# Kernel tuning notes

Hardware: AMD Instinct MI355X
Metric: run time of the kernel (lower is better)

Reference implementation:

```python
import jax, jax.numpy as jnp
import numpy as np

N_NODES = 50000
N_EDGES = 1600000
IN_F = 128
HID = 256
DROP_P = 0.6  # keep prob 0.4


def setup_inputs() -> dict:
    key = jax.random.key(0)
    ks = jax.random.split(key, 8)
    s_in = 1.0 / np.sqrt(IN_F)
    s_h = 1.0 / np.sqrt(HID)
    return {
        "x": jax.random.normal(ks[0], (N_NODES, IN_F), dtype=jnp.float32),
        "edge_index": jax.random.randint(ks[1], (2, N_EDGES), 0, N_NODES, dtype=jnp.int64),
        "w_rel0": jax.random.normal(ks[2], (IN_F, HID), dtype=jnp.float32) * s_in,
        "b_rel0": jax.random.normal(ks[3], (HID,), dtype=jnp.float32) * s_in,
        "w_root0": jax.random.normal(ks[4], (IN_F, HID), dtype=jnp.float32) * s_in,
        "w_rel1": jax.random.normal(ks[5], (HID, HID), dtype=jnp.float32) * s_h,
        "b_rel1": jax.random.normal(ks[6], (HID,), dtype=jnp.float32) * s_h,
        "w_root1": jax.random.normal(ks[7], (HID, HID), dtype=jnp.float32) * s_h,
    }


def _dropout(h, key, p):
    keep = 1.0 - p
    mask = jax.random.bernoulli(key, keep, h.shape)
    return jnp.where(mask, h / keep, 0.0).astype(h.dtype)


def _graph_conv(h, src, dst, n_nodes, w_rel, b_rel, w_root):
    # PyG GraphConv: out_i = lin_rel(sum_{j->i} x_j) + lin_root(x_i)
    agg = jax.ops.segment_sum(h[src], dst, num_segments=n_nodes)  # [N, F]
    return agg @ w_rel + b_rel + h @ w_root


def reference(x, edge_index, w_rel0, b_rel0, w_root0, w_rel1, b_rel1, w_root1):
    src, dst = edge_index[0], edge_index[1]  # flow: source -> target
    n = x.shape[0]
    dkey = jax.random.key(42)
    k0, k1 = jax.random.split(dkey)

    h = _dropout(x, k0, DROP_P)
    h = _graph_conv(h, src, dst, n, w_rel0, b_rel0, w_root0)
    h = jax.nn.relu(h)

    h = _dropout(h, k1, DROP_P)
    h = _graph_conv(h, src, dst, n, w_rel1, b_rel1, w_root1)
    h = jax.nn.relu(h)
    return h
```

## Files before the change

### kernel.cpp

```cpp
#include <hip/hip_runtime.h>
#include <cstdint>

typedef unsigned int u32;
typedef unsigned short u16;

#define NN 50000
#define NE 1600000
#define LDA0 288

#define NPART 196
#define SPAN1 2048
#define NB1 ((NE + SPAN1 - 1) / SPAN1)

typedef __bf16 bf16x8 __attribute__((ext_vector_type(8)));
typedef float f32x16 __attribute__((ext_vector_type(16)));

__host__ __device__ static inline void tf2x32(u32 ka, u32 kb, u32 x0, u32 x1,
                                              u32& o0, u32& o1) {
  const u32 kc = ka ^ kb ^ 0x1BD11BDAu;
  u32 v0 = x0 + ka, v1 = x1 + kb;
#define TFR(r) { v0 += v1; v1 = (v1 << (r)) | (v1 >> (32 - (r))); v1 ^= v0; }
  TFR(13) TFR(15) TFR(26) TFR(6)   v0 += kb; v1 += kc + 1u;
  TFR(17) TFR(29) TFR(16) TFR(24)  v0 += kc; v1 += ka + 2u;
  TFR(13) TFR(15) TFR(26) TFR(6)   v0 += ka; v1 += kb + 3u;
  TFR(17) TFR(29) TFR(16) TFR(24)  v0 += kb; v1 += kc + 4u;
  TFR(13) TFR(15) TFR(26) TFR(6)   v0 += kc; v1 += ka + 5u;
#undef TFR
  o0 = v0; o1 = v1;
}

__device__ static inline u32 tfbits(u32 ka, u32 kb, u32 j) {
  u32 o0, o1;
  tf2x32(ka, kb, 0u, j, o0, o1);
  return o0 ^ o1;
}

__device__ static inline float u01(u32 bits) {
  return __uint_as_float((bits >> 9) | 0x3f800000u) - 1.0f;
}
__device__ static inline u16 f2bf(float f) {
  u32 u = __float_as_uint(f);
  return (u16)((u + 0x7fffu + ((u >> 16) & 1u)) >> 16);
}
__device__ static inline float bflo(u32 w) { return __uint_as_float(w << 16); }
__device__ static inline float bfhi(u32 w) { return __uint_as_float(w & 0xffff0000u); }

#define PRO_DROP 12500
#define PRO_COMP 18750
#define PRO_TOT  19518

__global__ __launch_bounds__(256) void prologue_kernel(
    const float* __restrict__ x, const int* __restrict__ ei,
    const float* __restrict__ wr0, const float* __restrict__ wroot0,
    const float* __restrict__ wr1, const float* __restrict__ wroot1,
    u16* __restrict__ A0, u32* __restrict__ epack,
    u16* __restrict__ Wt0, u16* __restrict__ Wt1,
    u32 ka, u32 kb) {
  int bid = blockIdx.x;
  int tid = threadIdx.x;
  if (bid < PRO_DROP) {
    int j0 = (bid * 256 + tid) * 2;
    float v0 = (u01(tfbits(ka, kb, (u32)j0)) < 0.4f) ? x[j0] * 2.5f : 0.0f;
    float v1 = (u01(tfbits(ka, kb, (u32)j0 + 1u)) < 0.4f) ? x[j0 + 1] * 2.5f : 0.0f;
    int r = j0 >> 7, c = j0 & 127;
    *(u32*)&A0[r * LDA0 + 128 + c] = (u32)f2bf(v0) | ((u32)f2bf(v1) << 16);
  } else if (bid < PRO_COMP) {
    __shared__ int s_nz;
    if (tid == 0) s_nz = 0;
    __syncthreads();
    if (ei[2 * (tid & 127) + 1] != 0) s_nz = 1;
    __syncthreads();
    int f = s_nz ? 0 : 1;
    int i = (bid - PRO_DROP) * 256 + tid;
    int s = f ? ei[2 * (size_t)i] : ei[i];
    int d = f ? ei[2 * ((size_t)NE + i)] : ei[(size_t)NE + i];
    epack[i] = (u32)s | ((u32)d << 16);
  } else {
    int i = (bid - PRO_COMP) * 256 + tid;
    if (i < 256 * 256) {
      int n = i >> 8, k = i & 255;
      float v = (k < 128) ? wr0[k * 256 + n] : wroot0[(k - 128) * 256 + n];
      Wt0[n * 256 + k] = f2bf(v);
    }
    int j = i - 256 * 256;
    if (j >= 0 && j < 256 * 512) {
      int n = j >> 9, k = j & 511;
      float v = (k < 256) ? wr1[k * 256 + n] : wroot1[(k - 256) * 256 + n];
      Wt1[n * 512 + k] = f2bf(v);
    }
  }
}

__global__ __launch_bounds__(256) void p1_count_kernel(const u32* __restrict__ epack,
                                                       u32* __restrict__ pcnt) {
  __shared__ u32 cnt[NPART];
  int b = blockIdx.x, t = threadIdx.x;
  if (t < NPART) cnt[t] = 0;
  __syncthreads();
  int base = b * SPAN1;
#pragma unroll
  for (int k = 0; k < SPAN1 / 256; k++) {
    int i = base + k * 256 + t;
    if (i < NE) atomicAdd(&cnt[epack[i] >> 24], 1);
  }
  __syncthreads();
  if (t < NPART) pcnt[b * NPART + t] = cnt[t];
}

__global__ __launch_bounds__(256) void p1b_scan_kernel(const u32* __restrict__ pcnt,
                                                       u32* __restrict__ pofs,
                                                       u32* __restrict__ psize) {
  __shared__ u32 sc[256];
  int p = blockIdx.x, t = threadIdx.x;
  u32 val[4];
  u32 tsum = 0;
#pragma unroll
  for (int k = 0; k < 4; k++) {
    int b = t * 4 + k;
    val[k] = (b < NB1) ? pcnt[b * NPART + p] : 0;
    tsum += val[k];
  }
  sc[t] = tsum;
  __syncthreads();
#pragma unroll
  for (int d = 1; d < 256; d <<= 1) {
    u32 x = (t >= d) ? sc[t - d] : 0;
    __syncthreads();
    sc[t] += x;
    __syncthreads();
  }
  u32 run = sc[t] - tsum;
#pragma unroll
  for (int k = 0; k < 4; k++) {
    int b = t * 4 + k;
    if (b < NB1) { pofs[p * NB1 + b] = run; run += val[k]; }
  }
  if (t == 255) psize[p] = sc[255];
}

__global__ __launch_bounds__(256) void p1c_base_kernel(const u32* __restrict__ psize,
                                                       u32* __restrict__ pbase) {
  __shared__ u32 sc[256];
  int t = threadIdx.x;
  u32 v = (t < NPART) ? psize[t] : 0;
  sc[t] = v;
  __syncthreads();
#pragma unroll
  for (int d = 1; d < 256; d <<= 1) {
    u32 x = (t >= d) ? sc[t - d] : 0;
    __syncthreads();
    sc[t] += x;
    __syncthreads();
  }
  if (t < NPART) pbase[t] = sc[t] - v;
  if (t == NPART - 1) pbase[NPART] = sc[t];
}

__global__ __launch_bounds__(256) void p1d_pscatter_kernel(const u32* __restrict__ epack,
                                                           const u32* __restrict__ pofs,
                                                           const u32* __restrict__ pbase,
                                                           u32* __restrict__ part_buf) {
  __shared__ u32 cur[NPART];
  int b = blockIdx.x, t = threadIdx.x;
  if (t < NPART) cur[t] = pbase[t] + pofs[t * NB1 + b];
  __syncthreads();
  int base = b * SPAN1;
#pragma unroll
  for (int k = 0; k < SPAN1 / 256; k++) {
    int i = base + k * 256 + t;
    if (i < NE) {
      u32 v = epack[i];
      u32 p = v >> 24;
      u32 slot = atomicAdd(&cur[p], 1);
      part_buf[slot] = (v & 0xffffu) | (((v >> 16) & 255u) << 16);
    }
  }
}

__global__ __launch_bounds__(256) void p2_sort_kernel(const u32* __restrict__ part_buf,
                                                      const u32* __restrict__ pbase,
                                                      int* __restrict__ offs,
                                                      u16* __restrict__ ssrc) {
  __shared__ u32 cnt[256], sc[256], cur[256];
  int p = blockIdx.x, t = threadIdx.x;
  u32 pb = pbase[p];
  int sz = (int)(pbase[p + 1] - pb);
  cnt[t] = 0;
  __syncthreads();
  for (int i = t; i < sz; i += 256)
    atomicAdd(&cnt[(part_buf[pb + i] >> 16) & 255u], 1);
  __syncthreads();
  u32 val = cnt[t];
  sc[t] = val;
  __syncthreads();
#pragma unroll
  for (int d = 1; d < 256; d <<= 1) {
    u32 x = (t >= d) ? sc[t - d] : 0;
    __syncthreads();
    sc[t] += x;
    __syncthreads();
  }
  u32 excl = sc[t] - val;
  int node = (p << 8) + t;
  if (node <= NN) offs[node] = (int)(pb + excl);
  cur[t] = excl;
  __syncthreads();
  for (int i = t; i < sz; i += 256) {
    u32 v = part_buf[pb + i];
    u32 slot = atomicAdd(&cur[(v >> 16) & 255u], 1);
    ssrc[pb + slot] = (u16)(v & 0xffffu);
  }
}

#define ACC8Q(V, S) { acc[0] += rintf(bflo(V.x) * S); acc[1] += rintf(bfhi(V.x) * S); \
                      acc[2] += rintf(bflo(V.y) * S); acc[3] += rintf(bfhi(V.y) * S); \
                      acc[4] += rintf(bflo(V.z) * S); acc[5] += rintf(bfhi(V.z) * S); \
                      acc[6] += rintf(bflo(V.w) * S); acc[7] += rintf(bfhi(V.w) * S); }

__global__ __launch_bounds__(256) void agg0_kernel(u16* __restrict__ A0,
                                                   const int* __restrict__ offs,
                                                   const u16* __restrict__ ssrc) {
  const float S = 8192.0f, INV = 1.0f / 8192.0f;
  int node = blockIdx.x * 4 + (threadIdx.x >> 6);
  int lane = threadIdx.x & 63;
  int l15 = lane & 15, eh = lane >> 4;
  int s = offs[node], e = offs[node + 1];
  float acc[8] = {0.f, 0.f, 0.f, 0.f, 0.f, 0.f, 0.f, 0.f};
  int i = s;
  for (; i + 16 <= e; i += 16) {
    uint4 w0 = *(const uint4*)&A0[(int)ssrc[i + eh] * LDA0 + 128 + l15 * 8];
    uint4 w1 = *(const uint4*)&A0[(int)ssrc[i + 4 + eh] * LDA0 + 128 + l15 * 8];
    uint4 w2 = *(const uint4*)&A0[(int)ssrc[i + 8 + eh] * LDA0 + 128 + l15 * 8];
    uint4 w3 = *(const uint4*)&A0[(int)ssrc[i + 12 + eh] * LDA0 + 128 + l15 * 8];
    ACC8Q(w0, S); ACC8Q(w1, S); ACC8Q(w2, S); ACC8Q(w3, S);
  }
  for (; i + 4 <= e; i += 4) {
    uint4 w0 = *(const uint4*)&A0[(int)ssrc[i + eh] * LDA0 + 128 + l15 * 8];
    ACC8Q(w0, S);
  }
  if (i + eh < e) {
    uint4 w0 = *(const uint4*)&A0[(int)ssrc[i + eh] * LDA0 + 128 + l15 * 8];
    ACC8Q(w0, S);
  }
#pragma unroll
  for (int j = 0; j < 8; j++) {
    acc[j] += __shfl_xor(acc[j], 16);
    acc[j] += __shfl_xor(acc[j], 32);
  }
  if (lane < 16) {
    uint4 o;
    o.x = (u32)f2bf(acc[0] * INV) | ((u32)f2bf(acc[1] * INV) << 16);
    o.y = (u32)f2bf(acc[2] * INV) | ((u32)f2bf(acc[3] * INV) << 16);
    o.z = (u32)f2bf(acc[4] * INV) | ((u32)f2bf(acc[5] * INV) << 16);
    o.w = (u32)f2bf(acc[6] * INV) | ((u32)f2bf(acc[7] * INV) << 16);
    *(uint4*)&A0[node * LDA0 + l15 * 8] = o;
  }
}

__global__ __launch_bounds__(256) void agg1_kernel(u16* __restrict__ A1,
                                                   const int* __restrict__ offs,
                                                   const u16* __restrict__ ssrc,
                                                   int node0) {
  const float S = 256.0f, INV = 1.0f / 256.0f;
  int node = node0 + blockIdx.x * 4 + (threadIdx.x >> 6);
  int lane = threadIdx.x & 63;
  int l31 = lane & 31, eh = lane >> 5;
  int s = offs[node], e = offs[node + 1];
  float acc[8] = {0.f, 0.f, 0.f, 0.f, 0.f, 0.f, 0.f, 0.f};
  int i = s;
  for (; i + 8 <= e; i += 8) {
    uint4 w0 = *(const uint4*)&A1[(int)ssrc[i + eh] * 512 + 256 + l31 * 8];
    uint4 w1 = *(const uint4*)&A1[(int)ssrc[i + 2 + eh] * 512 + 256 + l31 * 8];
    uint4 w2 = *(const uint4*)&A1[(int)ssrc[i + 4 + eh] * 512 + 256 + l31 * 8];
    uint4 w3 = *(const uint4*)&A1[(int)ssrc[i + 6 + eh] * 512 + 256 + l31 * 8];
    ACC8Q(w0, S); ACC8Q(w1, S); ACC8Q(w2, S); ACC8Q(w3, S);
  }
  for (; i + 2 <= e; i += 2) {
    uint4 w0 = *(const uint4*)&A1[(int)ssrc[i + eh] * 512 + 256 + l31 * 8];
    ACC8Q(w0, S);
  }
  if (i + eh < e) {
    uint4 w0 = *(const uint4*)&A1[(int)ssrc[i + eh] * 512 + 256 + l31 * 8];
    ACC8Q(w0, S);
  }
#pragma unroll
  for (int j = 0; j < 8; j++) acc[j] += __shfl_xor(acc[j], 32);
  if (eh == 0) {
    uint4 o;
    o.x = (u32)f2bf(acc[0] * INV) | ((u32)f2bf(acc[1] * INV) << 16);
    o.y = (u32)f2bf(acc[2] * INV) | ((u32)f2bf(acc[3] * INV) << 16);
    o.z = (u32)f2bf(acc[4] * INV) | ((u32)f2bf(acc[5] * INV) << 16);
    o.w = (u32)f2bf(acc[6] * INV) | ((u32)f2bf(acc[7] * INV) << 16);
    *(uint4*)&A1[node * 512 + l31 * 8] = o;
  }
}

template <int K, int LDA, bool DROP>
__global__ __launch_bounds__(512) void gemm_kernel(const u16* __restrict__ A,
                                                   const u16* __restrict__ Wt,
                                                   const float* __restrict__ bias,
                                                   u16* __restrict__ outB,
                                                   float* __restrict__ outF,
                                                   u32 ka, u32 kb) {
  constexpr int BK = 64;
  constexpr int LDP = BK + 8;
  __shared__ __align__(16) u16 Alds[128 * LDP];
  __shared__ __align__(16) u16 Blds[256 * LDP];
  const int tid = threadIdx.x;
  const int row0 = blockIdx.x * 128;
  const int lane = tid & 63;
  const int wid = tid >> 6;
  const int wr = wid & 3;
  const int wc = wid >> 2;
  const int l31 = lane & 31;
  const int lkhi = (lane >> 5) * 8;

  f32x16 acc[4];
#pragma unroll
  for (int i = 0; i < 4; i++)
#pragma unroll
    for (int j = 0; j < 16; j++) acc[i][j] = 0.0f;

#pragma unroll
  for (int kc = 0; kc < K / BK; kc++) {
#pragma unroll
    for (int i = 0; i < 2; i++) {
      int id = tid + i * 512;
      int r = id >> 3, c = id & 7;
      int rg = row0 + r; if (rg > NN - 1) rg = NN - 1;
      *(uint4*)&Alds[r * LDP + c * 8] =
          *(const uint4*)&A[(size_t)rg * LDA + kc * BK + c * 8];
    }
#pragma unroll
    for (int i = 0; i < 4; i++) {
      int id = tid + i * 512;
      int r = id >> 3, c = id & 7;
      *(uint4*)&Blds[r * LDP + c * 8] =
          *(const uint4*)&Wt[(size_t)r * K + kc * BK + c * 8];
    }
    __syncthreads();
#pragma unroll
    for (int ks = 0; ks < BK / 16; ks++) {
      bf16x8 a = *(const bf16x8*)&Alds[(wr * 32 + l31) * LDP + ks * 16 + lkhi];
#pragma unroll
      for (int ct = 0; ct < 4; ct++) {
        bf16x8 b = *(const bf16x8*)&Blds[(wc * 128 + ct * 32 + l31) * LDP + ks * 16 + lkhi];
        acc[ct] = __builtin_amdgcn_mfma_f32_32x32x16_bf16(a, b, acc[ct], 0, 0, 0);
      }
    }
    __syncthreads();
  }

#pragma unroll
  for (int ct = 0; ct < 4; ct++) {
    int col = wc * 128 + ct * 32 + l31;
    float bv = bias[col];
#pragma unroll
    for (int r = 0; r < 16; r++) {
      int row = row0 + wr * 32 + (r & 3) + 8 * (r >> 2) + 4 * (lane >> 5);
      if (row < NN) {
        float v = acc[ct][r] + bv;
        v = fmaxf(v, 0.0f);
        if constexpr (DROP) {
          u32 j = (u32)row * 256u + (u32)col;
          v = (u01(tfbits(ka, kb, j)) < 0.4f) ? v * 2.5f : 0.0f;
          outB[(size_t)row * 512 + 256 + col] = f2bf(v);
        } else {
          outF[(size_t)row * 256 + col] = v;
        }
      }
    }
  }
}

extern "C" void kernel_launch(void* const* d_in, const int* in_sizes, int n_in,
                              void* d_out, int out_size, void* d_ws, size_t ws_size,
                              hipStream_t stream) {
  (void)in_sizes; (void)n_in; (void)out_size; (void)ws_size;
  const float* x       = (const float*)d_in[0];
  const int*   ei      = (const int*)d_in[1];
  const float* w_rel0  = (const float*)d_in[2];
  const float* b_rel0  = (const float*)d_in[3];
  const float* w_root0 = (const float*)d_in[4];
  const float* w_rel1  = (const float*)d_in[5];
  const float* b_rel1  = (const float*)d_in[6];
  const float* w_root1 = (const float*)d_in[7];
  float* out = (float*)d_out;

  u32 k0a, k0b, k1a, k1b;
  tf2x32(0u, 42u, 0u, 0u, k0a, k0b);
  tf2x32(0u, 42u, 0u, 1u, k1a, k1b);

  uint8_t* p = (uint8_t*)d_ws;
  auto alloc = [&](size_t bytes) {
    uint8_t* r = p;
    p += (bytes + 255) & ~(size_t)255;
    return r;
  };
  u16* A0       = (u16*)alloc((size_t)NN * LDA0 * 2);
  u16* Wt0      = (u16*)alloc(256 * 256 * 2);
  u16* Wt1      = (u16*)alloc(256 * 512 * 2);
  int* offs     = (int*)alloc((size_t)(NN + 1) * 4);
  u16* ssrc     = (u16*)alloc((size_t)NE * 2);
  u32* epack    = (u32*)alloc((size_t)NE * 4);
  u32* pcnt     = (u32*)alloc((size_t)NB1 * NPART * 4);
  u32* pofs     = (u32*)alloc((size_t)NPART * NB1 * 4);
  u32* psize    = (u32*)alloc((size_t)NPART * 4);
  u32* pbase    = (u32*)alloc((size_t)(NPART + 1) * 4);
  u32* part_buf = (u32*)alloc((size_t)NE * 4);

  u16* A1 = (u16*)d_out;

  const int GEMM_NB = (NN + 127) / 128;

  prologue_kernel<<<PRO_TOT, 256, 0, stream>>>(x, ei, w_rel0, w_root0, w_rel1,
                                               w_root1, A0, epack, Wt0, Wt1,
                                               k0a, k0b);
  p1_count_kernel<<<NB1, 256, 0, stream>>>(epack, pcnt);
  p1b_scan_kernel<<<NPART, 256, 0, stream>>>(pcnt, pofs, psize);
  p1c_base_kernel<<<1, 256, 0, stream>>>(psize, pbase);
  p1d_pscatter_kernel<<<NB1, 256, 0, stream>>>(epack, pofs, pbase, part_buf);
  p2_sort_kernel<<<NPART, 256, 0, stream>>>(part_buf, pbase, offs, ssrc);
  agg0_kernel<<<12500, 256, 0, stream>>>(A0, offs, ssrc);
  gemm_kernel<256, LDA0, true><<<GEMM_NB, 512, 0, stream>>>(A0, Wt0, b_rel0, A1, nullptr, k1a, k1b);
  agg1_kernel<<<6250, 256, 0, stream>>>(A1, offs, ssrc, 0);
  agg1_kernel<<<6250, 256, 0, stream>>>(A1, offs, ssrc, 25000);
  gemm_kernel<512, 512, false><<<GEMM_NB, 512, 0, stream>>>(A1, Wt1, b_rel1, nullptr, out, 0u, 0u);
}
```

Measured before the change: 308.0 us.

## Fold partition base scan into consumers, merge agg1 launches, widen GEMM row tile

The separate single-block base-scan kernel is removed. Instead, the scatter kernel and the sort kernel each recompute the prefix scan of partition sizes in shared memory, which drops one launch and its serial dependency at the cost of a redundant 256-wide scan in every block. The two half-range agg1 launches become one launch over all nodes. The GEMM tile grows from 128 to 256 rows, with each of the 8 waves now computing 32 rows across all 256 columns; this halves how often the weight tile is reloaded but cuts the grid to 196 blocks, which may underfill the GPU's CUs.

```diff
diff --git a/kernel.cpp b/kernel.cpp
--- a/kernel.cpp
+++ b/kernel.cpp
@@ -138,10 +138,13 @@
   if (t == 255) psize[p] = sc[255];
 }
 
-__global__ __launch_bounds__(256) void p1c_base_kernel(const u32* __restrict__ psize,
-                                                       u32* __restrict__ pbase) {
+__global__ __launch_bounds__(256) void p1d_pscatter_kernel(const u32* __restrict__ epack,
+                                                           const u32* __restrict__ pofs,
+                                                           const u32* __restrict__ psize,
+                                                           u32* __restrict__ part_buf) {
   __shared__ u32 sc[256];
-  int t = threadIdx.x;
+  __shared__ u32 cur[NPART];
+  int b = blockIdx.x, t = threadIdx.x;
   u32 v = (t < NPART) ? psize[t] : 0;
   sc[t] = v;
   __syncthreads();
@@ -152,41 +155,43 @@
     sc[t] += x;
     __syncthreads();
   }
-  if (t < NPART) pbase[t] = sc[t] - v;
-  if (t == NPART - 1) pbase[NPART] = sc[t];
-}
-
-__global__ __launch_bounds__(256) void p1d_pscatter_kernel(const u32* __restrict__ epack,
-                                                           const u32* __restrict__ pofs,
-                                                           const u32* __restrict__ pbase,
-                                                           u32* __restrict__ part_buf) {
-  __shared__ u32 cur[NPART];
-  int b = blockIdx.x, t = threadIdx.x;
-  if (t < NPART) cur[t] = pbase[t] + pofs[t * NB1 + b];
+  if (t < NPART) cur[t] = (sc[t] - v) + pofs[t * NB1 + b];
   __syncthreads();
   int base = b * SPAN1;
 #pragma unroll
   for (int k = 0; k < SPAN1 / 256; k++) {
     int i = base + k * 256 + t;
     if (i < NE) {
-      u32 v = epack[i];
-      u32 p = v >> 24;
+      u32 e = epack[i];
+      u32 p = e >> 24;
       u32 slot = atomicAdd(&cur[p], 1);
-      part_buf[slot] = (v & 0xffffu) | (((v >> 16) & 255u) << 16);
+      part_buf[slot] = (e & 0xffffu) | (((e >> 16) & 255u) << 16);
     }
   }
 }
 
 __global__ __launch_bounds__(256) void p2_sort_kernel(const u32* __restrict__ part_buf,
-                                                      const u32* __restrict__ pbase,
+                                                      const u32* __restrict__ psize,
                                                       int* __restrict__ offs,
                                                       u16* __restrict__ ssrc) {
-  __shared__ u32 cnt[256], sc[256], cur[256];
+  __shared__ u32 sc[256], cnt[256], cur[256];
+  __shared__ u32 s_pb;
   int p = blockIdx.x, t = threadIdx.x;
-  u32 pb = pbase[p];
-  int sz = (int)(pbase[p + 1] - pb);
+  u32 v = (t < NPART) ? psize[t] : 0;
+  sc[t] = v;
+  __syncthreads();
+#pragma unroll
+  for (int d = 1; d < 256; d <<= 1) {
+    u32 x = (t >= d) ? sc[t - d] : 0;
+    __syncthreads();
+    sc[t] += x;
+    __syncthreads();
+  }
+  if (t == p) s_pb = sc[t] - v;
   cnt[t] = 0;
   __syncthreads();
+  u32 pb = s_pb;
+  int sz = (int)psize[p];
   for (int i = t; i < sz; i += 256)
     atomicAdd(&cnt[(part_buf[pb + i] >> 16) & 255u], 1);
   __syncthreads();
@@ -206,9 +211,9 @@
   cur[t] = excl;
   __syncthreads();
   for (int i = t; i < sz; i += 256) {
-    u32 v = part_buf[pb + i];
-    u32 slot = atomicAdd(&cur[(v >> 16) & 255u], 1);
-    ssrc[pb + slot] = (u16)(v & 0xffffu);
+    u32 w = part_buf[pb + i];
+    u32 slot = atomicAdd(&cur[(w >> 16) & 255u], 1);
+    ssrc[pb + slot] = (u16)(w & 0xffffu);
   }
 }
 
@@ -259,10 +264,9 @@
 
 __global__ __launch_bounds__(256) void agg1_kernel(u16* __restrict__ A1,
                                                    const int* __restrict__ offs,
-                                                   const u16* __restrict__ ssrc,
-                                                   int node0) {
+                                                   const u16* __restrict__ ssrc) {
   const float S = 256.0f, INV = 1.0f / 256.0f;
-  int node = node0 + blockIdx.x * 4 + (threadIdx.x >> 6);
+  int node = blockIdx.x * 4 + (threadIdx.x >> 6);
   int lane = threadIdx.x & 63;
   int l31 = lane & 31, eh = lane >> 5;
   int s = offs[node], e = offs[node + 1];
@@ -304,27 +308,25 @@
                                                    u32 ka, u32 kb) {
   constexpr int BK = 64;
   constexpr int LDP = BK + 8;
-  __shared__ __align__(16) u16 Alds[128 * LDP];
+  __shared__ __align__(16) u16 Alds[256 * LDP];
   __shared__ __align__(16) u16 Blds[256 * LDP];
   const int tid = threadIdx.x;
-  const int row0 = blockIdx.x * 128;
+  const int row0 = blockIdx.x * 256;
   const int lane = tid & 63;
   const int wid = tid >> 6;
-  const int wr = wid & 3;
-  const int wc = wid >> 2;
   const int l31 = lane & 31;
   const int lkhi = (lane >> 5) * 8;
 
-  f32x16 acc[4];
-#pragma unroll
-  for (int i = 0; i < 4; i++)
+  f32x16 acc[8];
+#pragma unroll
+  for (int i = 0; i < 8; i++)
 #pragma unroll
     for (int j = 0; j < 16; j++) acc[i][j] = 0.0f;
 
 #pragma unroll
   for (int kc = 0; kc < K / BK; kc++) {
 #pragma unroll
-    for (int i = 0; i < 2; i++) {
+    for (int i = 0; i < 4; i++) {
       int id = tid + i * 512;
       int r = id >> 3, c = id & 7;
       int rg = row0 + r; if (rg > NN - 1) rg = NN - 1;
@@ -341,10 +343,10 @@
     __syncthreads();
 #pragma unroll
     for (int ks = 0; ks < BK / 16; ks++) {
-      bf16x8 a = *(const bf16x8*)&Alds[(wr * 32 + l31) * LDP + ks * 16 + lkhi];
-#pragma unroll
-      for (int ct = 0; ct < 4; ct++) {
-        bf16x8 b = *(const bf16x8*)&Blds[(wc * 128 + ct * 32 + l31) * LDP + ks * 16 + lkhi];
+      bf16x8 a = *(const bf16x8*)&Alds[(wid * 32 + l31) * LDP + ks * 16 + lkhi];
+#pragma unroll
+      for (int ct = 0; ct < 8; ct++) {
+        bf16x8 b = *(const bf16x8*)&Blds[(ct * 32 + l31) * LDP + ks * 16 + lkhi];
         acc[ct] = __builtin_amdgcn_mfma_f32_32x32x16_bf16(a, b, acc[ct], 0, 0, 0);
       }
     }
@@ -352,12 +354,12 @@
   }
 
 #pragma unroll
-  for (int ct = 0; ct < 4; ct++) {
-    int col = wc * 128 + ct * 32 + l31;
+  for (int ct = 0; ct < 8; ct++) {
+    int col = ct * 32 + l31;
     float bv = bias[col];
 #pragma unroll
     for (int r = 0; r < 16; r++) {
-      int row = row0 + wr * 32 + (r & 3) + 8 * (r >> 2) + 4 * (lane >> 5);
+      int row = row0 + wid * 32 + (r & 3) + 8 * (r >> 2) + 4 * (lane >> 5);
       if (row < NN) {
         float v = acc[ct][r] + bv;
         v = fmaxf(v, 0.0f);
@@ -406,24 +408,21 @@
   u32* pcnt     = (u32*)alloc((size_t)NB1 * NPART * 4);
   u32* pofs     = (u32*)alloc((size_t)NPART * NB1 * 4);
   u32* psize    = (u32*)alloc((size_t)NPART * 4);
-  u32* pbase    = (u32*)alloc((size_t)(NPART + 1) * 4);
   u32* part_buf = (u32*)alloc((size_t)NE * 4);
 
   u16* A1 = (u16*)d_out;
 
-  const int GEMM_NB = (NN + 127) / 128;
+  const int GEMM_NB = (NN + 255) / 256;
 
   prologue_kernel<<<PRO_TOT, 256, 0, stream>>>(x, ei, w_rel0, w_root0, w_rel1,
                                                w_root1, A0, epack, Wt0, Wt1,
                                                k0a, k0b);
   p1_count_kernel<<<NB1, 256, 0, stream>>>(epack, pcnt);
   p1b_scan_kernel<<<NPART, 256, 0, stream>>>(pcnt, pofs, psize);
-  p1c_base_kernel<<<1, 256, 0, stream>>>(psize, pbase);
-  p1d_pscatter_kernel<<<NB1, 256, 0, stream>>>(epack, pofs, pbase, part_buf);
-  p2_sort_kernel<<<NPART, 256, 0, stream>>>(part_buf, pbase, offs, ssrc);
+  p1d_pscatter_kernel<<<NB1, 256, 0, stream>>>(epack, pofs, psize, part_buf);
+  p2_sort_kernel<<<NPART, 256, 0, stream>>>(part_buf, psize, offs, ssrc);
   agg0_kernel<<<12500, 256, 0, stream>>>(A0, offs, ssrc);
   gemm_kernel<256, LDA0, true><<<GEMM_NB, 512, 0, stream>>>(A0, Wt0, b_rel0, A1, nullptr, k1a, k1b);
-  agg1_kernel<<<6250, 256, 0, stream>>>(A1, offs, ssrc, 0);
-  agg1_kernel<<<6250, 256, 0, stream>>>(A1, offs, ssrc, 25000);
+  agg1_kernel<<<12500, 256, 0, stream>>>(A1, offs, ssrc);
   gemm_kernel<512, 512, false><<<GEMM_NB, 512, 0, stream>>>(A1, Wt1, b_rel1, nullptr, out, 0u, 0u);
 }
```

Result: slower. 371.2 us (+20.5%).
